# Optimization experiments

Measured on AMD Instinct MI355X. Metric: run time of the kernel, lower is better.

The kernel has to match this reference:

```python
import jax, jax.numpy as jnp
import numpy as np

HIDDEN = 1024
HEADS = 16
HEAD_DIM = HIDDEN // HEADS  # 64
MAX_SEQ = 2048


def _rope_tables():
    # RotaryEmbedding buffers: freqs_cos/sin of shape [max_seq_len, head_dim//2]
    inv_freq = 1.0 / (10000.0 ** (jnp.arange(0, HEAD_DIM, 2, dtype=jnp.float32) / HEAD_DIM))
    t = jnp.arange(MAX_SEQ, dtype=jnp.float32)
    freqs = t[:, None] * inv_freq[None, :]
    return jnp.cos(freqs), jnp.sin(freqs)


def setup_inputs() -> dict:
    key = jax.random.key(0)
    k1, k2, k3 = jax.random.split(key, 3)
    x = jax.random.normal(k1, (2, 2048, HIDDEN), dtype=jnp.float32)
    qkv_w = jax.random.normal(k2, (HIDDEN, 3 * HIDDEN), dtype=jnp.float32) * 0.02
    qkv_b = jnp.zeros((3 * HIDDEN,), dtype=jnp.float32)
    out_w = jax.random.normal(k3, (HIDDEN, HIDDEN), dtype=jnp.float32) * 0.02
    out_b = jnp.zeros((HIDDEN,), dtype=jnp.float32)
    return {"x": x, "qkv_w": qkv_w, "qkv_b": qkv_b, "out_w": out_w, "out_b": out_b}


def reference(x, qkv_w, qkv_b, out_w, out_b):
    b, s, _ = x.shape
    qkv = x @ qkv_w + qkv_b                                   # [b, s, 3*hidden]
    qkv = qkv.reshape(b, s, HEADS, 3 * HEAD_DIM).transpose(0, 2, 1, 3)  # [b, h, s, 3*hd]
    q, k, v = jnp.split(qkv, 3, axis=-1)                      # each [b, h, s, hd]

    # Faithful to source quirk: rotary() is called on [b, h, s, hd] tensors so
    # x.shape[1] == num_heads -> seq_pos = arange(num_heads); tables are indexed
    # by HEAD index and broadcast over the sequence axis.
    cos_tab, sin_tab = _rope_tables()
    cos = cos_tab[:HEADS][None, :, None, :]                   # [1, h, 1, hd/2]
    sin = sin_tab[:HEADS][None, :, None, :]

    def rot(u):
        u1 = u[..., : HEAD_DIM // 2]
        u2 = u[..., HEAD_DIM // 2 :]
        return jnp.concatenate([u1 * cos - u2 * sin, u2 * cos + u1 * sin], axis=-1)

    q = rot(q)
    k = rot(k)

    scores = jnp.einsum("bhqd,bhkd->bhqk", q, k) / (HEAD_DIM ** 0.5)  # [b, h, s, s]
    attn = jax.nn.softmax(scores.astype(jnp.float32), axis=-1).astype(scores.dtype)
    out = jnp.einsum("bhqk,bhkd->bhqd", attn, v)              # [b, h, s, hd]
    out = out.transpose(0, 2, 1, 3).reshape(b, s, HEADS * HEAD_DIM)
    return out @ out_w + out_b
```

## Files before the change

### kernel.cpp

```cpp
#include <hip/hip_runtime.h>
#include <hip/hip_bf16.h>
#include <cstdint>
#include <cstddef>

typedef float  f32x4  __attribute__((ext_vector_type(4)));
typedef __bf16 bf16x8 __attribute__((ext_vector_type(8)));
typedef __bf16 bf16x4 __attribute__((ext_vector_type(4)));

#define HIDDEN 1024
#define SEQ    2048
#define BATCH  2
#define NQKV   3072
#define MTOT   4096

__device__ __forceinline__ __bf16 f2bf(float f) {
  unsigned u = __builtin_bit_cast(unsigned, f);
  u += 0x7FFFu + ((u >> 16) & 1u);
  unsigned short s = (unsigned short)(u >> 16);
  return __builtin_bit_cast(__bf16, s);
}

__device__ __forceinline__ unsigned pk2(float a, float b) {
  unsigned ua = __builtin_bit_cast(unsigned, a) + 0x8000u;
  unsigned ub = __builtin_bit_cast(unsigned, b) + 0x8000u;
  return __builtin_amdgcn_perm(ub, ua, 0x07060302u);
}

__device__ __forceinline__ float fexp2(float x) {
#if __has_builtin(__builtin_amdgcn_exp2f)
  return __builtin_amdgcn_exp2f(x);
#else
  return exp2f(x);
#endif
}

__device__ __forceinline__ void async16(const void* g, void* l) {
  __builtin_amdgcn_global_load_lds((__attribute__((address_space(1))) void*)(g),
                                   (__attribute__((address_space(3))) void*)(l),
                                   16, 0, 0);
}

__global__ __launch_bounds__(256) void k_prep(const float* __restrict__ x,
                                              __bf16* __restrict__ xb,
                                              const float* __restrict__ qkv_w,
                                              __bf16* __restrict__ wqkT,
                                              const float* __restrict__ out_w,
                                              __bf16* __restrict__ woT) {
  __shared__ float tile[64][65];
  const int bid = blockIdx.x, t = threadIdx.x;
  if (bid < 4096) {
    int i = bid * 256 + t;
    float4 v = ((const float4*)x)[i];
    bf16x4 o;
    o[0] = f2bf(v.x); o[1] = f2bf(v.y); o[2] = f2bf(v.z); o[3] = f2bf(v.w);
    ((bf16x4*)xb)[i] = o;
    return;
  }
  const float* W; __bf16* WT; int N, bx, by;
  if (bid < 4864) { int g = bid - 4096; W = qkv_w; WT = wqkT; N = NQKV;  bx = g % 48; by = g / 48; }
  else            { int g = bid - 4864; W = out_w; WT = woT;  N = HIDDEN; bx = g % 16; by = g / 16; }
  const int K = HIDDEN;
  int tx = t & 63, ty = t >> 6;
  int n0 = bx * 64, k0 = by * 64;
#pragma unroll
  for (int r = 0; r < 16; r++) {
    int row = r * 4 + ty;
    tile[row][tx] = W[(size_t)(k0 + row) * N + n0 + tx];
  }
  __syncthreads();
#pragma unroll
  for (int i2 = 0; i2 < 2; i2++) {
    int cc = i2 * 256 + t;
    int n = cc >> 3, ch = cc & 7;
    bf16x8 o;
#pragma unroll
    for (int j = 0; j < 8; j++) o[j] = f2bf(tile[ch * 8 + j][n]);
    *(bf16x8*)(WT + (size_t)(n0 + n) * K + k0 + ch * 8) = o;
  }
}

template <int BF16OUT, int VFUSE>
__global__ __launch_bounds__(256) void k_gemm(const __bf16* __restrict__ A,
                                              const __bf16* __restrict__ BT,
                                              const float* __restrict__ bias,
                                              void* __restrict__ Cout,
                                              __bf16* __restrict__ vt,
                                              int M, int N, int K) {
  __shared__ __align__(16) __bf16 As[128 * 32];
  __shared__ __align__(16) __bf16 Bs[128 * 32];
  const int t = threadIdx.x;
  const int lane = t & 63, wv = t >> 6;
  const int ln = lane & 15, quad = lane >> 4;
  const int wm = (wv & 1) * 64, wn = (wv >> 1) * 64;
  const int m0 = blockIdx.y * 128, n0 = blockIdx.x * 128;

  const f32x4 zero4 = {0.f, 0.f, 0.f, 0.f};
  f32x4 acc[4][4];
#pragma unroll
  for (int i = 0; i < 4; i++)
#pragma unroll
    for (int j = 0; j < 4; j++) acc[i][j] = zero4;

  for (int k0 = 0; k0 < K; k0 += 32) {
    __syncthreads();
#pragma unroll
    for (int i = 0; i < 2; i++) {
      int tt = i * 256 + t;
      int row = tt >> 2, ch = tt & 3;
      async16(A  + (size_t)(m0 + row) * K + k0 + ch * 8, As + tt * 8);
      async16(BT + (size_t)(n0 + row) * K + k0 + ch * 8, Bs + tt * 8);
    }
    __syncthreads();
    bf16x8 af[4], bfr[4];
#pragma unroll
    for (int x = 0; x < 4; x++)
      af[x] = *(const bf16x8*)(As + (wm + x * 16 + ln) * 32 + quad * 8);
#pragma unroll
    for (int x = 0; x < 4; x++)
      bfr[x] = *(const bf16x8*)(Bs + (wn + x * 16 + ln) * 32 + quad * 8);
#pragma unroll
    for (int mt = 0; mt < 4; mt++)
#pragma unroll
      for (int nt = 0; nt < 4; nt++)
        acc[mt][nt] = __builtin_amdgcn_mfma_f32_16x16x32_bf16(af[mt], bfr[nt], acc[mt][nt], 0, 0, 0);
  }
  const float CE = 0.125f * 1.44269504089f;
#pragma unroll
  for (int nt = 0; nt < 4; nt++) {
    int g = n0 + wn + nt * 16;
    int col = g + ln;
    float bv = bias[col];
    int off = g % 192;
    if (!VFUSE || off < 128) {
      float scl = (VFUSE && off < 64) ? CE : 1.0f;
#pragma unroll
      for (int mt = 0; mt < 4; mt++) {
#pragma unroll
        for (int r = 0; r < 4; r++) {
          int row = m0 + wm + mt * 16 + quad * 4 + r;
          float v = (acc[mt][nt][r] + bv) * scl;
          if (BF16OUT) ((__bf16*)Cout)[(size_t)row * N + col] = f2bf(v);
          else         ((float*)Cout)[(size_t)row * N + col] = v;
        }
      }
    } else {
      int hg = g / 192;
      int d  = off - 128 + ln;
#pragma unroll
      for (int mt = 0; mt < 4; mt++) {
        int rowb = m0 + wm + mt * 16;
        int bb = rowb >> 11;
        int s  = rowb & 2047;
        int sblk = s >> 7;
        int blk  = (wm + mt * 16) >> 4;
        int p = (blk & 3) * 32 + quad * 8 + ((blk >> 2) << 2);
        uint2 o;
        o.x = pk2(acc[mt][nt][0] + bv, acc[mt][nt][1] + bv);
        o.y = pk2(acc[mt][nt][2] + bv, acc[mt][nt][3] + bv);
        *(uint2*)(vt + ((size_t)((bb * 16 + hg) * 64 + d)) * SEQ + sblk * 128 + p) = o;
      }
    }
  }
}

__global__ __launch_bounds__(512, 4) void k_attn(const __bf16* __restrict__ qkv,
                                                 const __bf16* __restrict__ vt,
                                                 __bf16* __restrict__ aout) {
  __shared__ __align__(16) __bf16 smem[32768];
  const int t = threadIdx.x;
  const int lane = t & 63, wv = t >> 6;
  const int ln = lane & 15, quad = lane >> 4;
  const int sw8 = (quad ^ ((ln >> 1) & 3)) * 8;

  int gid = blockIdx.x;
  int slot = gid & 7, j = gid >> 3;
  int bh = slot * 4 + (j >> 4);
  int qt0 = j & 15;
  const int b = bh >> 4, h = bh & 15;
  const int q0 = qt0 * 128;

  const __bf16* qbase = qkv + (size_t)b * SEQ * NQKV + h * 192;
  const __bf16* kbase = qbase + 64;
  const __bf16* vbase = vt + (size_t)bh * 64 * SEQ;

#pragma unroll
  for (int i = 0; i < 2; i++) {
    int tt = i * 512 + t;
    int hh = tt >> 9, row = (tt >> 2) & 127, ch = tt & 3;
    int chs = ch ^ ((row >> 1) & 3);
    async16(kbase + (size_t)row * NQKV + hh * 32 + chs * 8, smem + tt * 8);
  }
#pragma unroll
  for (int i = 0; i < 2; i++) {
    int tt = i * 512 + t;
    int c = tt >> 8, d = (tt >> 2) & 63, w = tt & 3;
    int ws = w ^ ((d >> 1) & 3);
    async16(vbase + (size_t)d * SEQ + c * 32 + ws * 8, smem + 16384 + tt * 8);
  }

  bf16x8 qf[2];
#pragma unroll
  for (int dc = 0; dc < 2; dc++)
    qf[dc] = *(const bf16x8*)(qbase + (size_t)(q0 + wv * 16 + ln) * NQKV + dc * 32 + quad * 8);

  const f32x4 zero4 = {0.f, 0.f, 0.f, 0.f};
  f32x4 O[4];
  f32x4 psumv = zero4;
#pragma unroll
  for (int dt = 0; dt < 4; dt++) O[dt] = zero4;

  for (int it = 0; it < SEQ / 128; it++) {
    __syncthreads();
    const __bf16* Ks = smem + (it & 1) * 8192;
    const __bf16* Vs = smem + 16384 + (it & 1) * 8192;
    if (it + 1 < SEQ / 128) {
      __bf16* Kd = smem + ((it + 1) & 1) * 8192;
      __bf16* Vd = smem + 16384 + ((it + 1) & 1) * 8192;
      const __bf16* kn = kbase + (size_t)(it + 1) * 128 * NQKV;
      const __bf16* vn = vbase + (it + 1) * 128;
#pragma unroll
      for (int i = 0; i < 2; i++) {
        int tt = i * 512 + t;
        int hh = tt >> 9, row = (tt >> 2) & 127, ch = tt & 3;
        int chs = ch ^ ((row >> 1) & 3);
        async16(kn + (size_t)row * NQKV + hh * 32 + chs * 8, Kd + tt * 8);
      }
#pragma unroll
      for (int i = 0; i < 2; i++) {
        int tt = i * 512 + t;
        int c = tt >> 8, d = (tt >> 2) & 63, w = tt & 3;
        int ws = w ^ ((d >> 1) & 3);
        async16(vn + (size_t)d * SEQ + c * 32 + ws * 8, Vd + tt * 8);
      }
    }

    unsigned Pp[8][2];
#pragma unroll
    for (int blk = 0; blk < 8; blk++) {
      bf16x8 kf0 = *(const bf16x8*)(Ks +        (blk * 16 + ln) * 32 + sw8);
      bf16x8 kf1 = *(const bf16x8*)(Ks + 4096 + (blk * 16 + ln) * 32 + sw8);
      f32x4 s = __builtin_amdgcn_mfma_f32_16x16x32_bf16(kf0, qf[0], zero4, 0, 0, 0);
      s = __builtin_amdgcn_mfma_f32_16x16x32_bf16(kf1, qf[1], s, 0, 0, 0);
      float p0 = fexp2(s[0]), p1 = fexp2(s[1]), p2 = fexp2(s[2]), p3 = fexp2(s[3]);
      psumv[0] += p0; psumv[1] += p1; psumv[2] += p2; psumv[3] += p3;
      Pp[blk][0] = pk2(p0, p1);
      Pp[blk][1] = pk2(p2, p3);
    }
#pragma unroll
    for (int kc = 0; kc < 4; kc++) {
      union { bf16x8 v; unsigned u[4]; } pf;
      pf.u[0] = Pp[kc][0]; pf.u[1] = Pp[kc][1];
      pf.u[2] = Pp[kc + 4][0]; pf.u[3] = Pp[kc + 4][1];
#pragma unroll
      for (int dt = 0; dt < 4; dt++) {
        bf16x8 vf = *(const bf16x8*)(Vs + kc * 2048 + (dt * 16 + ln) * 32 + sw8);
        O[dt] = __builtin_amdgcn_mfma_f32_16x16x32_bf16(pf.v, vf, O[dt], 0, 0, 0);
      }
    }
  }

  float l = psumv[0] + psumv[1] + psumv[2] + psumv[3];
  l += __shfl_xor(l, 16);
  l += __shfl_xor(l, 32);
  float inv = 1.0f / l;
  __bf16* stage = smem + wv * 1024;
#pragma unroll
  for (int r = 0; r < 4; r++) {
    float ir = __shfl(inv, quad * 4 + r);
#pragma unroll
    for (int dt = 0; dt < 4; dt++)
      stage[(quad * 4 + r) * 64 + dt * 16 + ln] = f2bf(O[dt][r] * ir);
  }
  __bf16* obase = aout + (size_t)(b * SEQ + q0 + wv * 16) * HIDDEN + h * 64;
#pragma unroll
  for (int i = 0; i < 2; i++) {
    int tt = i * 64 + lane; int row = tt >> 3, ch = tt & 7;
    *(bf16x8*)(obase + (size_t)row * HIDDEN + ch * 8) = *(const bf16x8*)(stage + row * 64 + ch * 8);
  }
}

extern "C" void kernel_launch(void* const* d_in, const int* in_sizes, int n_in,
                              void* d_out, int out_size, void* d_ws, size_t ws_size,
                              hipStream_t stream) {
  const float* x     = (const float*)d_in[0];
  const float* qkv_w = (const float*)d_in[1];
  const float* qkv_b = (const float*)d_in[2];
  const float* out_w = (const float*)d_in[3];
  const float* out_b = (const float*)d_in[4];

  char* ws = (char*)d_ws;
  __bf16* xb   = (__bf16*)(ws);
  __bf16* wqkT = (__bf16*)(ws + 8388608);
  __bf16* woT  = (__bf16*)(ws + 14680064);
  __bf16* qkv  = (__bf16*)(ws + 16777216);
  __bf16* vt   = (__bf16*)(ws + 41943040);
  __bf16* aout = (__bf16*)(ws + 50331648);

  k_prep<<<5120, 256, 0, stream>>>(x, xb, qkv_w, wqkT, out_w, woT);
  k_gemm<1, 1><<<dim3(NQKV / 128, MTOT / 128), 256, 0, stream>>>(xb, wqkT, qkv_b, qkv, vt, MTOT, NQKV, HIDDEN);
  k_attn<<<512, 512, 0, stream>>>(qkv, vt, aout);
  k_gemm<0, 0><<<dim3(HIDDEN / 128, MTOT / 128), 256, 0, stream>>>(aout, woT, out_b, (float*)d_out, nullptr, MTOT, HIDDEN, HIDDEN);
}
```

Baseline: 191.9 us.

## Shrink GEMM N-tile, swizzle LDS reads, compute softmax row sum via MFMA

```diff
diff --git a/kernel.cpp b/kernel.cpp
--- a/kernel.cpp
+++ b/kernel.cpp
@@ -80,26 +80,27 @@
 }
 
 template <int BF16OUT, int VFUSE>
-__global__ __launch_bounds__(256) void k_gemm(const __bf16* __restrict__ A,
-                                              const __bf16* __restrict__ BT,
-                                              const float* __restrict__ bias,
-                                              void* __restrict__ Cout,
-                                              __bf16* __restrict__ vt,
-                                              int M, int N, int K) {
+__global__ __launch_bounds__(256, 4) void k_gemm(const __bf16* __restrict__ A,
+                                                 const __bf16* __restrict__ BT,
+                                                 const float* __restrict__ bias,
+                                                 void* __restrict__ Cout,
+                                                 __bf16* __restrict__ vt,
+                                                 int M, int N, int K) {
   __shared__ __align__(16) __bf16 As[128 * 32];
-  __shared__ __align__(16) __bf16 Bs[128 * 32];
+  __shared__ __align__(16) __bf16 Bs[64 * 32];
   const int t = threadIdx.x;
   const int lane = t & 63, wv = t >> 6;
   const int ln = lane & 15, quad = lane >> 4;
-  const int wm = (wv & 1) * 64, wn = (wv >> 1) * 64;
-  const int m0 = blockIdx.y * 128, n0 = blockIdx.x * 128;
+  const int sw8 = (quad ^ ((ln >> 1) & 3)) * 8;
+  const int wm = (wv & 1) * 64, wn = (wv >> 1) * 32;
+  const int m0 = blockIdx.y * 128, n0 = blockIdx.x * 64;
 
   const f32x4 zero4 = {0.f, 0.f, 0.f, 0.f};
-  f32x4 acc[4][4];
+  f32x4 acc[4][2];
 #pragma unroll
   for (int i = 0; i < 4; i++)
 #pragma unroll
-    for (int j = 0; j < 4; j++) acc[i][j] = zero4;
+    for (int j = 0; j < 2; j++) acc[i][j] = zero4;
 
   for (int k0 = 0; k0 < K; k0 += 32) {
     __syncthreads();
@@ -107,26 +108,31 @@
     for (int i = 0; i < 2; i++) {
       int tt = i * 256 + t;
       int row = tt >> 2, ch = tt & 3;
-      async16(A  + (size_t)(m0 + row) * K + k0 + ch * 8, As + tt * 8);
-      async16(BT + (size_t)(n0 + row) * K + k0 + ch * 8, Bs + tt * 8);
+      int chs = ch ^ ((row >> 1) & 3);
+      async16(A + (size_t)(m0 + row) * K + k0 + chs * 8, As + tt * 8);
+    }
+    {
+      int row = t >> 2, ch = t & 3;
+      int chs = ch ^ ((row >> 1) & 3);
+      async16(BT + (size_t)(n0 + row) * K + k0 + chs * 8, Bs + t * 8);
     }
     __syncthreads();
-    bf16x8 af[4], bfr[4];
+    bf16x8 af[4], bfr[2];
 #pragma unroll
     for (int x = 0; x < 4; x++)
-      af[x] = *(const bf16x8*)(As + (wm + x * 16 + ln) * 32 + quad * 8);
-#pragma unroll
-    for (int x = 0; x < 4; x++)
-      bfr[x] = *(const bf16x8*)(Bs + (wn + x * 16 + ln) * 32 + quad * 8);
+      af[x] = *(const bf16x8*)(As + (wm + x * 16 + ln) * 32 + sw8);
+#pragma unroll
+    for (int x = 0; x < 2; x++)
+      bfr[x] = *(const bf16x8*)(Bs + (wn + x * 16 + ln) * 32 + sw8);
 #pragma unroll
     for (int mt = 0; mt < 4; mt++)
 #pragma unroll
-      for (int nt = 0; nt < 4; nt++)
+      for (int nt = 0; nt < 2; nt++)
         acc[mt][nt] = __builtin_amdgcn_mfma_f32_16x16x32_bf16(af[mt], bfr[nt], acc[mt][nt], 0, 0, 0);
   }
   const float CE = 0.125f * 1.44269504089f;
 #pragma unroll
-  for (int nt = 0; nt < 4; nt++) {
+  for (int nt = 0; nt < 2; nt++) {
     int g = n0 + wn + nt * 16;
     int col = g + ln;
     float bv = bias[col];
@@ -152,7 +158,7 @@
         int bb = rowb >> 11;
         int s  = rowb & 2047;
         int sblk = s >> 7;
-        int blk  = (wm + mt * 16) >> 4;
+        int blk  = (s >> 4) & 7;
         int p = (blk & 3) * 32 + quad * 8 + ((blk >> 2) << 2);
         uint2 o;
         o.x = pk2(acc[mt][nt][0] + bv, acc[mt][nt][1] + bv);
@@ -203,9 +209,12 @@
   for (int dc = 0; dc < 2; dc++)
     qf[dc] = *(const bf16x8*)(qbase + (size_t)(q0 + wv * 16 + ln) * NQKV + dc * 32 + quad * 8);
 
+  union { unsigned u[4]; bf16x8 v; } ones;
+  ones.u[0] = ones.u[1] = ones.u[2] = ones.u[3] = 0x3F803F80u;
+
   const f32x4 zero4 = {0.f, 0.f, 0.f, 0.f};
   f32x4 O[4];
-  f32x4 psumv = zero4;
+  f32x4 Ol = zero4;
 #pragma unroll
   for (int dt = 0; dt < 4; dt++) O[dt] = zero4;
 
@@ -241,16 +250,15 @@
       bf16x8 kf1 = *(const bf16x8*)(Ks + 4096 + (blk * 16 + ln) * 32 + sw8);
       f32x4 s = __builtin_amdgcn_mfma_f32_16x16x32_bf16(kf0, qf[0], zero4, 0, 0, 0);
       s = __builtin_amdgcn_mfma_f32_16x16x32_bf16(kf1, qf[1], s, 0, 0, 0);
-      float p0 = fexp2(s[0]), p1 = fexp2(s[1]), p2 = fexp2(s[2]), p3 = fexp2(s[3]);
-      psumv[0] += p0; psumv[1] += p1; psumv[2] += p2; psumv[3] += p3;
-      Pp[blk][0] = pk2(p0, p1);
-      Pp[blk][1] = pk2(p2, p3);
+      Pp[blk][0] = pk2(fexp2(s[0]), fexp2(s[1]));
+      Pp[blk][1] = pk2(fexp2(s[2]), fexp2(s[3]));
     }
 #pragma unroll
     for (int kc = 0; kc < 4; kc++) {
       union { bf16x8 v; unsigned u[4]; } pf;
       pf.u[0] = Pp[kc][0]; pf.u[1] = Pp[kc][1];
       pf.u[2] = Pp[kc + 4][0]; pf.u[3] = Pp[kc + 4][1];
+      Ol = __builtin_amdgcn_mfma_f32_16x16x32_bf16(pf.v, ones.v, Ol, 0, 0, 0);
 #pragma unroll
       for (int dt = 0; dt < 4; dt++) {
         bf16x8 vf = *(const bf16x8*)(Vs + kc * 2048 + (dt * 16 + ln) * 32 + sw8);
@@ -259,14 +267,10 @@
     }
   }
 
-  float l = psumv[0] + psumv[1] + psumv[2] + psumv[3];
-  l += __shfl_xor(l, 16);
-  l += __shfl_xor(l, 32);
-  float inv = 1.0f / l;
   __bf16* stage = smem + wv * 1024;
 #pragma unroll
   for (int r = 0; r < 4; r++) {
-    float ir = __shfl(inv, quad * 4 + r);
+    float ir = 1.0f / Ol[r];
 #pragma unroll
     for (int dt = 0; dt < 4; dt++)
       stage[(quad * 4 + r) * 64 + dt * 16 + ln] = f2bf(O[dt][r] * ir);
@@ -297,7 +301,7 @@
   __bf16* aout = (__bf16*)(ws + 50331648);
 
   k_prep<<<5120, 256, 0, stream>>>(x, xb, qkv_w, wqkT, out_w, woT);
-  k_gemm<1, 1><<<dim3(NQKV / 128, MTOT / 128), 256, 0, stream>>>(xb, wqkT, qkv_b, qkv, vt, MTOT, NQKV, HIDDEN);
+  k_gemm<1, 1><<<dim3(NQKV / 64, MTOT / 128), 256, 0, stream>>>(xb, wqkT, qkv_b, qkv, vt, MTOT, NQKV, HIDDEN);
   k_attn<<<512, 512, 0, stream>>>(qkv, vt, aout);
-  k_gemm<0, 0><<<dim3(HIDDEN / 128, MTOT / 128), 256, 0, stream>>>(aout, woT, out_b, (float*)d_out, nullptr, MTOT, HIDDEN, HIDDEN);
-}
+  k_gemm<0, 0><<<dim3(HIDDEN / 64, MTOT / 128), 256, 0, stream>>>(aout, woT, out_b, (float*)d_out, nullptr, MTOT, HIDDEN, HIDDEN);
+}
```

Result: no change. 188.5 us (-1.8%).
